# Performance work log

Measured on AMD Instinct MI355X. Metric: run time of the kernel, lower is better.

Reference implementation:

```python
import jax, jax.numpy as jnp
import numpy as np

B, N, H, HID, LOCALITY = 2, 4096, 4, 256, 30.0
VD = HID // H
F32_MAX = jnp.finfo(jnp.float32).max


def setup_inputs() -> dict:
    key = jax.random.key(0)
    k1, k2, k3, k4 = jax.random.split(key, 4)
    m_dist = jax.random.uniform(k1, (B, N, N), dtype=jnp.float32)  # pairwise distances (b,N,N)
    x = jax.random.normal(k2, (B, N, HID), dtype=jnp.float32)
    r = jax.random.normal(k3, (1, H, 1, 1), dtype=jnp.float32)  # learned per-head distance scale
    # lecun_normal: std = 1/sqrt(fan_in), fan_in = HID
    weight = jax.random.normal(k4, (H, HID, VD), dtype=jnp.float32) / np.sqrt(HID)
    return {"m_dist": m_dist, "x": x, "r": r, "weight": weight}


def reference(m_dist, x, r, weight):
    # scaled distance per head: (b,h,n,n)
    scaled = m_dist[:, None, :, :] * (r ** 2)
    # percentile-thresholded local mask (linear interpolation, per row)
    thresh = jnp.percentile(scaled, LOCALITY, axis=-1, keepdims=True, method="linear")
    scaled = jnp.where(scaled <= thresh, scaled, F32_MAX)
    att = jax.nn.softmax(-scaled, axis=-1)  # (b,h,n,n)
    value = jnp.einsum("bnj,hjk->bhnk", x, weight)  # (b,h,n,v)
    out = jnp.einsum("bhnj,bhjd->bhnd", att, value)  # (b,h,n,v)
    out = jnp.transpose(out, (0, 2, 1, 3)).reshape(out.shape[0], -1, HID)  # (b,n,hid)
    return jax.nn.gelu(out, approximate=False)
```

## Files before the change

### kernel.cpp

```cpp
#include <hip/hip_runtime.h>
#include <hip/hip_bf16.h>

#define Bc   2
#define Nc   4096
#define Hc   4
#define HIDc 256
#define VDc  64

typedef short s8v  __attribute__((ext_vector_type(8)));
typedef float f4v  __attribute__((ext_vector_type(4)));

static __device__ __forceinline__ unsigned short bf16bits(float f) {
    __hip_bfloat16 h = __float2bfloat16(f);
    return *(unsigned short*)&h;
}

__global__ __launch_bounds__(256) void prep_kernel(
    const float* __restrict__ x, const float* __restrict__ wgt,
    unsigned short* __restrict__ xh, unsigned short* __restrict__ xl,
    unsigned short* __restrict__ wh, unsigned short* __restrict__ wl)
{
    int t = threadIdx.x, bid = blockIdx.x;
    if (bid < 1024) {
        size_t g = ((size_t)bid * 256 + t) * 8;
        float4 v0 = *(const float4*)(x + g);
        float4 v1 = *(const float4*)(x + g + 4);
        float f[8] = {v0.x, v0.y, v0.z, v0.w, v1.x, v1.y, v1.z, v1.w};
        union { s8v v; unsigned short u[8]; } hs, ls;
        #pragma unroll
        for (int i = 0; i < 8; i++) {
            __hip_bfloat16 hb = __float2bfloat16(f[i]);
            float hf = __bfloat162float(hb);
            hs.u[i] = *(unsigned short*)&hb;
            ls.u[i] = bf16bits(f[i] - hf);
        }
        *(s8v*)(xh + g) = hs.v;
        *(s8v*)(xl + g) = ls.v;
    } else {
        int b2 = bid - 1024;
        int h  = b2 >> 5;
        int kt = (b2 >> 3) & 3;
        int jc = b2 & 7;
        int lane = t >> 2, ii = t & 3;
        #pragma unroll
        for (int u = 0; u < 2; u++) {
            int i = ii * 2 + u;
            int j = jc * 32 + (lane >> 4) * 8 + i;
            int k = kt * 16 + (lane & 15);
            float v = wgt[((size_t)h * HIDc + j) * VDc + k];
            __hip_bfloat16 hb = __float2bfloat16(v);
            float hf = __bfloat162float(hb);
            size_t o = ((((size_t)h * 4 + kt) * 8 + jc) * 64 + lane) * 8 + i;
            wh[o] = *(unsigned short*)&hb;
            wl[o] = bf16bits(v - hf);
        }
    }
}

__global__ __launch_bounds__(256) void value_kernel(
    const unsigned short* __restrict__ xh, const unsigned short* __restrict__ xl,
    const unsigned short* __restrict__ wh, const unsigned short* __restrict__ wl,
    unsigned short* __restrict__ vt_g)
{
    int t  = threadIdx.x;
    int bid = blockIdx.x;
    int nt = bid & 63;
    int h  = (bid >> 6) & 3;
    int b  = bid >> 8;
    int n0 = nt * 64;

    int w = t >> 6, lane = t & 63, q4 = lane >> 4, m16 = lane & 15;
    int nb = n0 + w * 16;

    const unsigned short* xhp = xh + ((size_t)(b * Nc + nb + m16)) * HIDc + q4 * 8;
    const unsigned short* xlp = xl + ((size_t)(b * Nc + nb + m16)) * HIDc + q4 * 8;

    f4v acc[4];
    #pragma unroll
    for (int kt = 0; kt < 4; kt++) acc[kt] = (f4v){0.f, 0.f, 0.f, 0.f};

    #pragma unroll
    for (int jc = 0; jc < 8; jc++) {
        s8v bh = *(const s8v*)(xhp + jc * 32);
        s8v bl = *(const s8v*)(xlp + jc * 32);
        #pragma unroll
        for (int kt = 0; kt < 4; kt++) {
            size_t ao = (((size_t)(h * 4 + kt) * 8 + jc) << 9) + lane * 8;
            s8v ah = *(const s8v*)(wh + ao);
            s8v al = *(const s8v*)(wl + ao);
            acc[kt] = __builtin_amdgcn_mfma_f32_16x16x32_bf16(ah, bh, acc[kt], 0, 0, 0);
            acc[kt] = __builtin_amdgcn_mfma_f32_16x16x32_bf16(al, bh, acc[kt], 0, 0, 0);
            acc[kt] = __builtin_amdgcn_mfma_f32_16x16x32_bf16(ah, bl, acc[kt], 0, 0, 0);
        }
    }

    unsigned short* vg = vt_g + (((size_t)b * Hc + h) * VDc) * Nc;
    #pragma unroll
    for (int kt = 0; kt < 4; kt++) {
        #pragma unroll
        for (int rg = 0; rg < 4; rg++) {
            int k = kt * 16 + q4 * 4 + rg;
            vg[(size_t)k * Nc + nb + m16] = bf16bits(acc[kt][rg]);
        }
    }
}

__global__ __launch_bounds__(256) void thresh_kernel(
    const float* __restrict__ m_dist,
    float* __restrict__ thr_out, float* __restrict__ min_out)
{
    __shared__ unsigned int hist[1024];
    __shared__ float wredf[4];
    __shared__ unsigned int wsum[4];
    __shared__ unsigned int wscan[4];
    __shared__ int b0s, b1s;
    __shared__ unsigned int c0s;
    __shared__ unsigned int ncand;
    __shared__ float cand[256];
    __shared__ float s0s, s1s;

    int t = threadIdx.x;
    size_t rowid = blockIdx.x;
    const float* row = m_dist + rowid * Nc;

    float4 vals[4];
    float lmin = 1e30f;
    #pragma unroll
    for (int i = 0; i < 4; i++) {
        float4 v = ((const float4*)row)[t + i * 256];
        vals[i] = v;
        lmin = fminf(lmin, fminf(fminf(v.x, v.y), fminf(v.z, v.w)));
    }
    #pragma unroll
    for (int o = 32; o > 0; o >>= 1) lmin = fminf(lmin, __shfl_xor(lmin, o));
    if ((t & 63) == 0) wredf[t >> 6] = lmin;

    const unsigned int R0 = 1228u, R1 = 1229u;
    float wlo = 0.25f, whi = 0.35f;
    int b0 = 0, b1 = 0;
    unsigned int C0 = 0;

    for (;;) {
        float wscale = 1024.0f / (whi - wlo);

        for (int i = t; i < 1024; i += 256) hist[i] = 0u;
        if (t == 0) ncand = 0u;
        __syncthreads();

        unsigned int cb = 0;
        #pragma unroll
        for (int i = 0; i < 4; i++) {
            float a[4] = {vals[i].x, vals[i].y, vals[i].z, vals[i].w};
            #pragma unroll
            for (int j = 0; j < 4; j++) {
                float v = a[j];
                if (v < wlo) {
                    cb++;
                } else {
                    int bx = (int)((v - wlo) * wscale);
                    if (bx < 1024) atomicAdd(&hist[bx], 1u);
                }
            }
        }
        #pragma unroll
        for (int o = 32; o > 0; o >>= 1) cb += __shfl_xor(cb, o);
        if ((t & 63) == 0) wsum[t >> 6] = cb;
        __syncthreads();
        unsigned int Cb = wsum[0] + wsum[1] + wsum[2] + wsum[3];

        unsigned int c[4], csum = 0;
        #pragma unroll
        for (int j = 0; j < 4; j++) { c[j] = hist[t * 4 + j]; csum += c[j]; }
        unsigned int inc = csum;
        #pragma unroll
        for (int o = 1; o < 64; o <<= 1) {
            unsigned int nv = __shfl_up(inc, o);
            if ((t & 63) >= o) inc += nv;
        }
        if ((t & 63) == 63) wscan[t >> 6] = inc;
        __syncthreads();
        unsigned int wpref = 0;
        for (int wv = 0; wv < (t >> 6); wv++) wpref += wscan[wv];
        unsigned int T = wscan[0] + wscan[1] + wscan[2] + wscan[3];
        unsigned int P = Cb + wpref + inc - csum;

        unsigned int cum = P;
        #pragma unroll
        for (int j = 0; j < 4; j++) {
            unsigned int lo = cum, hi = cum + c[j];
            if (R0 >= lo && R0 < hi) { b0s = t * 4 + j; c0s = lo; }
            if (R1 >= lo && R1 < hi) { b1s = t * 4 + j; }
            cum = hi;
        }
        __syncthreads();

        if (Cb <= R0 && R1 < Cb + T) { b0 = b0s; b1 = b1s; C0 = c0s; break; }
        wlo = 0.0f; whi = 1.001f;
    }

    float wscale = 1024.0f / (whi - wlo);
    #pragma unroll
    for (int i = 0; i < 4; i++) {
        float a[4] = {vals[i].x, vals[i].y, vals[i].z, vals[i].w};
        #pragma unroll
        for (int j = 0; j < 4; j++) {
            float v = a[j];
            if (v >= wlo) {
                int bx = (int)((v - wlo) * wscale);
                if (bx >= b0 && bx <= b1) {
                    unsigned int p = atomicAdd(&ncand, 1u);
                    if (p < 256u) cand[p] = v;
                }
            }
        }
    }
    __syncthreads();
    unsigned int nc = min(ncand, 256u);
    if ((unsigned int)t < nc) {
        float v = cand[t];
        unsigned int rk = C0;
        for (unsigned int j = 0; j < nc; j++) {
            float u = cand[j];
            rk += (u < v || (u == v && j < (unsigned int)t)) ? 1u : 0u;
        }
        if (rk == R0) s0s = v;
        if (rk == R1) s1s = v;
    }
    __syncthreads();
    if (t == 0) {
        thr_out[rowid] = 0.5f * (s0s + s1s);
        min_out[rowid] = fminf(fminf(wredf[0], wredf[1]), fminf(wredf[2], wredf[3]));
    }
}

#define NT 64
#define JT 64
#define BIGF 3.0e38f

__global__ __launch_bounds__(1024, 8) void attn_kernel(
    const float* __restrict__ m_dist, const float* __restrict__ rr,
    const unsigned short* __restrict__ vt_g,
    const float* __restrict__ thr_g, const float* __restrict__ min_g,
    float* __restrict__ Op, float* __restrict__ Zp, int jlen)
{
    __shared__ float ms[NT * 64];
    __shared__ unsigned short vt[Hc * VDc * 64];

    int t = threadIdx.x;
    const int nblk = Bc * (Nc / NT);
    int js = blockIdx.x / nblk;
    int rb = blockIdx.x - js * nblk;
    int b  = rb >> 6;
    int n0 = (rb & 63) * NT;
    int j0 = js * jlen;

    int lane = t & 63, q = lane >> 4, m16 = lane & 15;
    int w = t >> 6;
    int h = w & 3, rq = w >> 2;
    int row = rq * 16 + m16;

    float mn = min_g[b * Nc + n0 + row];
    float rv = rr[h];
    float cc = -(rv * rv) * 1.4426950408889634f;
    float nmncc = -mn * cc;

    f4v acc[4];
    #pragma unroll
    for (int ct = 0; ct < 4; ct++) acc[ct] = (f4v){0.f, 0.f, 0.f, 0.f};
    float zacc = 0.f;

    const float* mbase = m_dist + ((size_t)b * Nc + n0) * Nc + j0;
    const unsigned short* vtb = vt_g + ((size_t)b * Hc * VDc) * Nc + j0;

    int mrow = t >> 4, mch = t & 15;
    int msw  = mrow * 64 + ((mch ^ (mrow & 15)) << 2);
    float thm = thr_g[b * Nc + n0 + mrow];

    int schunk8 = ((t & 7) ^ ((t >> 3) & 7)) * 8;
    unsigned short* vt_wbase = &vt[(w * 8) * 64];

    int a00 = row * 64 + (((q * 2 + 0) ^ m16) << 2);
    int a01 = row * 64 + (((q * 2 + 1) ^ m16) << 2);
    int a10 = row * 64 + (((8 + q * 2 + 0) ^ m16) << 2);
    int a11 = row * 64 + (((8 + q * 2 + 1) ^ m16) << 2);

    for (int jt = 0; jt < jlen; jt += JT) {
        #pragma unroll
        for (int i = 0; i < 2; i++) {
            int rrow = (t >> 3) + i * 128;
            __builtin_amdgcn_global_load_lds(
                (const __attribute__((address_space(1))) void*)
                    (vtb + (size_t)rrow * Nc + jt + schunk8),
                (__attribute__((address_space(3))) void*)
                    (vt_wbase + i * 128 * 64),
                16, 0, 0);
        }
        {
            float4 v = *(const float4*)(mbase + (size_t)mrow * Nc + jt + mch * 4);
            v.x = (v.x <= thm) ? v.x : BIGF;
            v.y = (v.y <= thm) ? v.y : BIGF;
            v.z = (v.z <= thm) ? v.z : BIGF;
            v.w = (v.w <= thm) ? v.w : BIGF;
            *(float4*)&ms[msw] = v;
        }
        __syncthreads();

        const unsigned short* vb = &vt[(h * VDc) * 64];
        #pragma unroll
        for (int ks = 0; ks < 2; ks++) {
            float4 a0 = *(const float4*)&ms[ks ? a10 : a00];
            float4 a1 = *(const float4*)&ms[ks ? a11 : a01];
            float w0 = __builtin_amdgcn_exp2f(__builtin_fmaf(a0.x, cc, nmncc));
            float w1 = __builtin_amdgcn_exp2f(__builtin_fmaf(a0.y, cc, nmncc));
            float w2 = __builtin_amdgcn_exp2f(__builtin_fmaf(a0.z, cc, nmncc));
            float w3 = __builtin_amdgcn_exp2f(__builtin_fmaf(a0.w, cc, nmncc));
            float w4 = __builtin_amdgcn_exp2f(__builtin_fmaf(a1.x, cc, nmncc));
            float w5 = __builtin_amdgcn_exp2f(__builtin_fmaf(a1.y, cc, nmncc));
            float w6 = __builtin_amdgcn_exp2f(__builtin_fmaf(a1.z, cc, nmncc));
            float w7 = __builtin_amdgcn_exp2f(__builtin_fmaf(a1.w, cc, nmncc));
            zacc += ((w0 + w1) + (w2 + w3)) + ((w4 + w5) + (w6 + w7));
            union { s8v v; __hip_bfloat162 h2[4]; } afu;
            afu.h2[0] = __float22bfloat162_rn((float2){w0, w1});
            afu.h2[1] = __float22bfloat162_rn((float2){w2, w3});
            afu.h2[2] = __float22bfloat162_rn((float2){w4, w5});
            afu.h2[3] = __float22bfloat162_rn((float2){w6, w7});
            #pragma unroll
            for (int ct = 0; ct < 4; ct++) {
                int brow = ct * 16 + m16;
                s8v bf = *(const s8v*)(vb + brow * 64 + (((ks * 4 + q) ^ (m16 & 7)) << 3));
                acc[ct] = __builtin_amdgcn_mfma_f32_16x16x32_bf16(afu.v, bf, acc[ct], 0, 0, 0);
            }
        }
        __syncthreads();
    }

    zacc += __shfl_xor(zacc, 16);
    zacc += __shfl_xor(zacc, 32);
    if (q == 0)
        Zp[(((size_t)js * Bc + b) * Hc + h) * Nc + n0 + row] = zacc;

    #pragma unroll
    for (int ct = 0; ct < 4; ct++) {
        #pragma unroll
        for (int rg = 0; rg < 4; rg++) {
            int nl = rq * 16 + q * 4 + rg;
            Op[(((size_t)js * Bc + b) * Nc + n0 + nl) * HIDc + h * VDc + ct * 16 + m16]
                = acc[ct][rg];
        }
    }
}

__global__ __launch_bounds__(256) void combine_kernel(
    const float* __restrict__ Op, const float* __restrict__ Zp,
    float* __restrict__ out, int S)
{
    int g = blockIdx.x * 256 + threadIdx.x;
    int c4 = g & 63;
    int n  = (g >> 6) & (Nc - 1);
    int b  = g >> 18;
    int h  = c4 >> 4;

    float z = 0.f;
    float4 v = {0.f, 0.f, 0.f, 0.f};
    for (int s = 0; s < S; s++) {
        z += Zp[(((size_t)s * Bc + b) * Hc + h) * Nc + n];
        float4 p = *(const float4*)&Op[(((size_t)s * Bc + b) * Nc + n) * HIDc + c4 * 4];
        v.x += p.x; v.y += p.y; v.z += p.z; v.w += p.w;
    }
    float iz = 1.0f / z;
    float4 o;
    float u;
    u = v.x * iz; o.x = 0.5f * u * (1.0f + erff(u * 0.7071067811865476f));
    u = v.y * iz; o.y = 0.5f * u * (1.0f + erff(u * 0.7071067811865476f));
    u = v.z * iz; o.z = 0.5f * u * (1.0f + erff(u * 0.7071067811865476f));
    u = v.w * iz; o.w = 0.5f * u * (1.0f + erff(u * 0.7071067811865476f));
    *(float4*)&out[(((size_t)b * Nc + n) * HIDc) + c4 * 4] = o;
}

extern "C" void kernel_launch(void* const* d_in, const int* in_sizes, int n_in,
                              void* d_out, int out_size, void* d_ws, size_t ws_size,
                              hipStream_t stream) {
    const float* m_dist = (const float*)d_in[0];
    const float* x      = (const float*)d_in[1];
    const float* r      = (const float*)d_in[2];
    const float* weight = (const float*)d_in[3];
    float* out = (float*)d_out;

    char* ws = (char*)d_ws;
    const size_t MB = 1024 * 1024;
    unsigned short* vt = (unsigned short*)ws;
    float* thr = (float*)(ws + 4 * MB);
    float* mn  = (float*)(ws + 4 * MB + 32 * 1024);
    float* Zp  = (float*)(ws + 4 * MB + 64 * 1024);
    float* Op  = (float*)(ws + 5 * MB);

    int S = 4;
    if (ws_size < 14 * MB + 4 * (size_t)(Bc * Nc * HIDc * 4)) S = 2;
    if (ws_size < 14 * MB + 2 * (size_t)(Bc * Nc * HIDc * 4)) S = 1;
    int jlen = Nc / S;

    char* pb = ws + 5 * MB + (size_t)S * (Bc * Nc * HIDc * 4);
    unsigned short* xh = (unsigned short*)pb;
    unsigned short* xl = (unsigned short*)(pb + 4 * MB);
    unsigned short* wh = (unsigned short*)(pb + 8 * MB);
    unsigned short* wl = (unsigned short*)(pb + 8 * MB + 128 * 1024);

    prep_kernel<<<1152, 256, 0, stream>>>(x, weight, xh, xl, wh, wl);
    value_kernel<<<512, 256, 0, stream>>>(xh, xl, wh, wl, vt);
    thresh_kernel<<<Bc * Nc, 256, 0, stream>>>(m_dist, thr, mn);
    attn_kernel<<<S * Bc * (Nc / NT), 1024, 0, stream>>>(m_dist, r, vt, thr, mn, Op, Zp, jlen);
    combine_kernel<<<(Bc * Nc * HIDc) / 1024, 256, 0, stream>>>(Op, Zp, out, S);
}
```

Measured before the change: 266.8 us.

## Fuse weight prep into threshold kernel and split x to bf16 inside value kernel

Weight bf16 hi/lo splitting now runs as extra blocks of the threshold kernel, so one launch is removed. The x hi/lo split is done on the fly in the value kernel, which removes the xh/xl intermediate buffers and their global write and read traffic. The attention inner MFMA section is also wrapped in s_setprio to raise wave priority during compute. Workspace requirements shrink accordingly. Value blocks now redo the x conversion per head (4x redundant conversion work).

```diff
diff --git a/kernel.cpp b/kernel.cpp
--- a/kernel.cpp
+++ b/kernel.cpp
@@ -15,32 +15,17 @@
     return *(unsigned short*)&h;
 }
 
-__global__ __launch_bounds__(256) void prep_kernel(
-    const float* __restrict__ x, const float* __restrict__ wgt,
-    unsigned short* __restrict__ xh, unsigned short* __restrict__ xl,
-    unsigned short* __restrict__ wh, unsigned short* __restrict__ wl)
+__global__ __launch_bounds__(256) void front_kernel(
+    const float* __restrict__ m_dist, const float* __restrict__ wgt,
+    unsigned short* __restrict__ wh, unsigned short* __restrict__ wl,
+    float* __restrict__ thr_out, float* __restrict__ min_out)
 {
     int t = threadIdx.x, bid = blockIdx.x;
-    if (bid < 1024) {
-        size_t g = ((size_t)bid * 256 + t) * 8;
-        float4 v0 = *(const float4*)(x + g);
-        float4 v1 = *(const float4*)(x + g + 4);
-        float f[8] = {v0.x, v0.y, v0.z, v0.w, v1.x, v1.y, v1.z, v1.w};
-        union { s8v v; unsigned short u[8]; } hs, ls;
-        #pragma unroll
-        for (int i = 0; i < 8; i++) {
-            __hip_bfloat16 hb = __float2bfloat16(f[i]);
-            float hf = __bfloat162float(hb);
-            hs.u[i] = *(unsigned short*)&hb;
-            ls.u[i] = bf16bits(f[i] - hf);
-        }
-        *(s8v*)(xh + g) = hs.v;
-        *(s8v*)(xl + g) = ls.v;
-    } else {
-        int b2 = bid - 1024;
-        int h  = b2 >> 5;
-        int kt = (b2 >> 3) & 3;
-        int jc = b2 & 7;
+
+    if (bid < 128) {
+        int h  = bid >> 5;
+        int kt = (bid >> 3) & 3;
+        int jc = bid & 7;
         int lane = t >> 2, ii = t & 3;
         #pragma unroll
         for (int u = 0; u < 2; u++) {
@@ -54,61 +39,9 @@
             wh[o] = *(unsigned short*)&hb;
             wl[o] = bf16bits(v - hf);
         }
-    }
-}
-
-__global__ __launch_bounds__(256) void value_kernel(
-    const unsigned short* __restrict__ xh, const unsigned short* __restrict__ xl,
-    const unsigned short* __restrict__ wh, const unsigned short* __restrict__ wl,
-    unsigned short* __restrict__ vt_g)
-{
-    int t  = threadIdx.x;
-    int bid = blockIdx.x;
-    int nt = bid & 63;
-    int h  = (bid >> 6) & 3;
-    int b  = bid >> 8;
-    int n0 = nt * 64;
-
-    int w = t >> 6, lane = t & 63, q4 = lane >> 4, m16 = lane & 15;
-    int nb = n0 + w * 16;
-
-    const unsigned short* xhp = xh + ((size_t)(b * Nc + nb + m16)) * HIDc + q4 * 8;
-    const unsigned short* xlp = xl + ((size_t)(b * Nc + nb + m16)) * HIDc + q4 * 8;
-
-    f4v acc[4];
-    #pragma unroll
-    for (int kt = 0; kt < 4; kt++) acc[kt] = (f4v){0.f, 0.f, 0.f, 0.f};
-
-    #pragma unroll
-    for (int jc = 0; jc < 8; jc++) {
-        s8v bh = *(const s8v*)(xhp + jc * 32);
-        s8v bl = *(const s8v*)(xlp + jc * 32);
-        #pragma unroll
-        for (int kt = 0; kt < 4; kt++) {
-            size_t ao = (((size_t)(h * 4 + kt) * 8 + jc) << 9) + lane * 8;
-            s8v ah = *(const s8v*)(wh + ao);
-            s8v al = *(const s8v*)(wl + ao);
-            acc[kt] = __builtin_amdgcn_mfma_f32_16x16x32_bf16(ah, bh, acc[kt], 0, 0, 0);
-            acc[kt] = __builtin_amdgcn_mfma_f32_16x16x32_bf16(al, bh, acc[kt], 0, 0, 0);
-            acc[kt] = __builtin_amdgcn_mfma_f32_16x16x32_bf16(ah, bl, acc[kt], 0, 0, 0);
-        }
-    }
-
-    unsigned short* vg = vt_g + (((size_t)b * Hc + h) * VDc) * Nc;
-    #pragma unroll
-    for (int kt = 0; kt < 4; kt++) {
-        #pragma unroll
-        for (int rg = 0; rg < 4; rg++) {
-            int k = kt * 16 + q4 * 4 + rg;
-            vg[(size_t)k * Nc + nb + m16] = bf16bits(acc[kt][rg]);
-        }
-    }
-}
-
-__global__ __launch_bounds__(256) void thresh_kernel(
-    const float* __restrict__ m_dist,
-    float* __restrict__ thr_out, float* __restrict__ min_out)
-{
+        return;
+    }
+
     __shared__ unsigned int hist[1024];
     __shared__ float wredf[4];
     __shared__ unsigned int wsum[4];
@@ -119,8 +52,7 @@
     __shared__ float cand[256];
     __shared__ float s0s, s1s;
 
-    int t = threadIdx.x;
-    size_t rowid = blockIdx.x;
+    size_t rowid = bid - 128;
     const float* row = m_dist + rowid * Nc;
 
     float4 vals[4];
@@ -233,6 +165,62 @@
     }
 }
 
+__global__ __launch_bounds__(256) void value_kernel(
+    const float* __restrict__ x,
+    const unsigned short* __restrict__ wh, const unsigned short* __restrict__ wl,
+    unsigned short* __restrict__ vt_g)
+{
+    int t  = threadIdx.x;
+    int bid = blockIdx.x;
+    int nt = bid & 63;
+    int h  = (bid >> 6) & 3;
+    int b  = bid >> 8;
+    int n0 = nt * 64;
+
+    int w = t >> 6, lane = t & 63, q4 = lane >> 4, m16 = lane & 15;
+    int nb = n0 + w * 16;
+
+    const float* xp = x + ((size_t)(b * Nc + nb + m16)) * HIDc + q4 * 8;
+
+    f4v acc[4];
+    #pragma unroll
+    for (int kt = 0; kt < 4; kt++) acc[kt] = (f4v){0.f, 0.f, 0.f, 0.f};
+
+    #pragma unroll
+    for (int jc = 0; jc < 8; jc++) {
+        float4 xv0 = *(const float4*)(xp + jc * 32);
+        float4 xv1 = *(const float4*)(xp + jc * 32 + 4);
+        float f[8] = {xv0.x, xv0.y, xv0.z, xv0.w, xv1.x, xv1.y, xv1.z, xv1.w};
+        union { s8v v; unsigned short u[8]; } hs, ls;
+        #pragma unroll
+        for (int i = 0; i < 8; i++) {
+            __hip_bfloat16 hb = __float2bfloat16(f[i]);
+            float hf = __bfloat162float(hb);
+            hs.u[i] = *(unsigned short*)&hb;
+            ls.u[i] = bf16bits(f[i] - hf);
+        }
+        #pragma unroll
+        for (int kt = 0; kt < 4; kt++) {
+            size_t ao = (((size_t)(h * 4 + kt) * 8 + jc) << 9) + lane * 8;
+            s8v ah = *(const s8v*)(wh + ao);
+            s8v al = *(const s8v*)(wl + ao);
+            acc[kt] = __builtin_amdgcn_mfma_f32_16x16x32_bf16(ah, hs.v, acc[kt], 0, 0, 0);
+            acc[kt] = __builtin_amdgcn_mfma_f32_16x16x32_bf16(al, hs.v, acc[kt], 0, 0, 0);
+            acc[kt] = __builtin_amdgcn_mfma_f32_16x16x32_bf16(ah, ls.v, acc[kt], 0, 0, 0);
+        }
+    }
+
+    unsigned short* vg = vt_g + (((size_t)b * Hc + h) * VDc) * Nc;
+    #pragma unroll
+    for (int kt = 0; kt < 4; kt++) {
+        #pragma unroll
+        for (int rg = 0; rg < 4; rg++) {
+            int k = kt * 16 + q4 * 4 + rg;
+            vg[(size_t)k * Nc + nb + m16] = bf16bits(acc[kt][rg]);
+        }
+    }
+}
+
 #define NT 64
 #define JT 64
 #define BIGF 3.0e38f
@@ -305,6 +293,7 @@
         }
         __syncthreads();
 
+        __builtin_amdgcn_s_setprio(1);
         const unsigned short* vb = &vt[(h * VDc) * 64];
         #pragma unroll
         for (int ks = 0; ks < 2; ks++) {
@@ -331,6 +320,7 @@
                 acc[ct] = __builtin_amdgcn_mfma_f32_16x16x32_bf16(afu.v, bf, acc[ct], 0, 0, 0);
             }
         }
+        __builtin_amdgcn_s_setprio(0);
         __syncthreads();
     }
 
@@ -394,20 +384,18 @@
     float* Zp  = (float*)(ws + 4 * MB + 64 * 1024);
     float* Op  = (float*)(ws + 5 * MB);
 
+    const size_t OpSz = (size_t)Bc * Nc * HIDc * 4;
     int S = 4;
-    if (ws_size < 14 * MB + 4 * (size_t)(Bc * Nc * HIDc * 4)) S = 2;
-    if (ws_size < 14 * MB + 2 * (size_t)(Bc * Nc * HIDc * 4)) S = 1;
+    if (ws_size < 6 * MB + 4 * OpSz) S = 2;
+    if (ws_size < 6 * MB + 2 * OpSz) S = 1;
     int jlen = Nc / S;
 
-    char* pb = ws + 5 * MB + (size_t)S * (Bc * Nc * HIDc * 4);
-    unsigned short* xh = (unsigned short*)pb;
-    unsigned short* xl = (unsigned short*)(pb + 4 * MB);
-    unsigned short* wh = (unsigned short*)(pb + 8 * MB);
-    unsigned short* wl = (unsigned short*)(pb + 8 * MB + 128 * 1024);
-
-    prep_kernel<<<1152, 256, 0, stream>>>(x, weight, xh, xl, wh, wl);
-    value_kernel<<<512, 256, 0, stream>>>(xh, xl, wh, wl, vt);
-    thresh_kernel<<<Bc * Nc, 256, 0, stream>>>(m_dist, thr, mn);
+    char* pb = ws + 5 * MB + (size_t)S * OpSz;
+    unsigned short* wh = (unsigned short*)pb;
+    unsigned short* wl = (unsigned short*)(pb + 128 * 1024);
+
+    front_kernel<<<128 + Bc * Nc, 256, 0, stream>>>(m_dist, weight, wh, wl, thr, mn);
+    value_kernel<<<512, 256, 0, stream>>>(x, wh, wl, vt);
     attn_kernel<<<S * Bc * (Nc / NT), 1024, 0, stream>>>(m_dist, r, vt, thr, mn, Op, Zp, jlen);
     combine_kernel<<<(Bc * Nc * HIDc) / 1024, 256, 0, stream>>>(Op, Zp, out, S);
 }
```

Result: no change. 266.4 us (-0.2%).
